# Performance work log

Hardware: AMD Instinct MI355X
Metric: run time of the kernel (lower is better)

Reference implementation:

```python
import jax, jax.numpy as jnp
import numpy as np

B, H, W, C = 4, 64, 64, 256


def _conv1x1(t, w, b):
    # 1x1 Conv2D == per-pixel matmul over channels (NHWC)
    return jnp.einsum('bhwc,cd->bhwd', t, w) + b


def setup_inputs() -> dict:
    key = jax.random.key(0)
    ks = jax.random.split(key, 12)
    s = 0.02
    inp = {
        'x': jax.random.normal(ks[0], (B, H, W, C), dtype=jnp.float32),
        'g': jax.random.normal(ks[1], (B, H, W, C), dtype=jnp.float32),
        'Wx1': jax.random.normal(ks[2], (C, C), dtype=jnp.float32) * s,
        'bx1': jnp.zeros((C,), dtype=jnp.float32),
        'Wx2': jax.random.normal(ks[3], (C, C), dtype=jnp.float32) * s,
        'bx2': jnp.zeros((C,), dtype=jnp.float32),
        'Wx3': jax.random.normal(ks[4], (C, C), dtype=jnp.float32) * s,
        'bx3': jnp.zeros((C,), dtype=jnp.float32),
        'Wg1': jax.random.normal(ks[5], (C, C), dtype=jnp.float32) * s,
        'bg1': jnp.zeros((C,), dtype=jnp.float32),
        'Wg2': jax.random.normal(ks[6], (C, C), dtype=jnp.float32) * s,
        'bg2': jnp.zeros((C,), dtype=jnp.float32),
    }
    return inp


def reference(x, g, Wx1, bx1, Wx2, bx2, Wx3, bx3, Wg1, bg1, Wg2, bg2):
    b, h, w, c = x.shape
    hw = h * w
    # x-branch projections, flattened to (B, HW, C)
    xw1 = _conv1x1(x, Wx1, bx1).reshape(b, hw, c)
    xw2 = _conv1x1(x, Wx2, bx2).reshape(b, hw, c)
    xw3 = _conv1x1(x, Wx3, bx3).reshape(b, hw, c)
    # g-branch projections
    gw1 = _conv1x1(g, Wg1, bg1).reshape(b, hw, c)
    gw2 = _conv1x1(g, Wg2, bg2).reshape(b, hw, c)
    # Dot(axes=(2,1))([xw_2, xw_1^T]) -> (B, HW, HW), softmax over last axis
    x_attn = jax.nn.softmax(jnp.einsum('bic,bjc->bij', xw2, xw1), axis=-1)
    g_attn = jax.nn.softmax(jnp.einsum('bic,bjc->bij', gw2, gw1), axis=-1)
    # elementwise gate then renormalize
    attn = jax.nn.softmax(x_attn * g_attn, axis=-1)
    # Keras Dot(axes=1): contract axis 1 of attn with axis 1 of xw3
    # out[b, j, c] = sum_i attn[b, i, j] * xw3[b, i, c]
    out = jnp.einsum('bij,bic->bjc', attn, xw3).reshape(b, h, w, c)
    return x + out
```

## Files before the change

### kernel.cpp

```cpp
#include <hip/hip_runtime.h>

typedef float f32x4 __attribute__((ext_vector_type(4)));
typedef short s16x8 __attribute__((ext_vector_type(8)));
typedef unsigned char u8;
typedef unsigned short u16;
typedef unsigned int u32;
typedef unsigned long long u64;

#define NPOS 4096
#define CCH  256
#define MTOT 16384
#define PBYTES ((size_t)NPOS * NPOS * 2)

#define SZ_F8   ((size_t)MTOT * 256)
#define O_F8    ((size_t)0)
#define O_WT    (O_F8   + 4 * SZ_F8)
#define O_XW3T  (O_WT   + (size_t)5*256*256*2)
#define O_XW3S  (O_XW3T + (size_t)MTOT*256*2)
#define O_ZX    (O_XW3S + (size_t)MTOT*256*2)
#define O_ZG    (O_ZX   + (size_t)8*MTOT*4)
#define O_ID    (O_ZG   + (size_t)8*MTOT*4)
#define O_Z2    (O_ID   + (size_t)MTOT*4)
#define O_IZ2   (O_Z2   + (size_t)8*MTOT*4)
#define O_P     (O_IZ2  + (size_t)MTOT*4)

__device__ __forceinline__ u16 f2bf(float f) {
    u32 u = __builtin_bit_cast(u32, f);
    u32 r = (u + 0x7FFFu + ((u >> 16) & 1u)) >> 16;
    return (u16)r;
}
__device__ __forceinline__ float bf2f(u16 h) {
    u32 u = ((u32)h) << 16;
    return __builtin_bit_cast(float, u);
}
__device__ __forceinline__ f32x4 mfma_bf16(s16x8 a, s16x8 b, f32x4 c) {
    return __builtin_amdgcn_mfma_f32_16x16x32_bf16(a, b, c, 0, 0, 0);
}
__device__ __forceinline__ f32x4 mfma_fp8(long a, long b, f32x4 c) {
    return __builtin_amdgcn_mfma_f32_16x16x32_fp8_fp8(a, b, c, 0, 0, 0);
}
__device__ __forceinline__ int xcd_swz(int bid, int nwg) {
    return (bid & 7) * (nwg >> 3) + (bid >> 3);
}

__global__ __launch_bounds__(256) void prep_w(
    const float* __restrict__ W0, const float* __restrict__ W1,
    const float* __restrict__ W2, const float* __restrict__ W3,
    const float* __restrict__ W4, u32* __restrict__ wT)
{
    const int p = blockIdx.x, kq = blockIdx.y, n = threadIdx.x;
    const float* W = (p==0)?W0:(p==1)?W1:(p==2)?W2:(p==3)?W3:W4;
#pragma unroll 4
    for (int kk = 0; kk < 32; ++kk) {
        int k = kq*64 + kk*2;
        float v0 = W[k*256 + n];
        float v1 = W[(k+1)*256 + n];
        wT[(p*65536 + n*256 + k) >> 1] = (u32)f2bf(v0) | ((u32)f2bf(v1) << 16);
    }
}

__global__ __launch_bounds__(256) void proj_kernel(
    const float* __restrict__ x, const float* __restrict__ g,
    const float* __restrict__ bb0, const float* __restrict__ bb1,
    const float* __restrict__ bb2, const float* __restrict__ bb3,
    const float* __restrict__ bb4,
    const u16* __restrict__ wT, u8* __restrict__ f8, u8* __restrict__ xw3T)
{
    const int branch = blockIdx.y;
    const int m0 = blockIdx.x * 128;
    const float* A = branch ? g : x;
    __shared__ u8 sA[128*512];
    __shared__ u8 sC[128*512];
    const int t = threadIdx.x;
    const int l = t & 63, lr = l & 15, lg = l >> 4;
    const int wv = t >> 6, wm = wv >> 1, wn = wv & 1;

    {
        const int m = t >> 1, h = t & 1;
        const float* src = &A[(size_t)(m0 + m) * 256 + h * 128];
        const u32 dbase = m * 512;
#pragma unroll
        for (int c = 0; c < 16; ++c) {
            float4 a = *(const float4*)(src + c*8);
            float4 b = *(const float4*)(src + c*8 + 4);
            u32 pk[4] = { (u32)f2bf(a.x) | ((u32)f2bf(a.y)<<16),
                          (u32)f2bf(a.z) | ((u32)f2bf(a.w)<<16),
                          (u32)f2bf(b.x) | ((u32)f2bf(b.y)<<16),
                          (u32)f2bf(b.z) | ((u32)f2bf(b.w)<<16) };
            int kbyte = h*256 + c*16;
            *(uint4*)&sA[dbase + (kbyte ^ ((m & 7) << 4))] = *(uint4*)pk;
        }
    }
    __syncthreads();

    const int np = branch ? 2 : 3;
    for (int pp = 0; pp < np; ++pp) {
        const int p = branch ? 3 + pp : pp;
        const float* bias = (p==0)?bb0:(p==1)?bb1:(p==2)?bb2:(p==3)?bb3:bb4;
        f32x4 acc[4][8];
#pragma unroll
        for (int i = 0; i < 4; ++i)
#pragma unroll
            for (int j = 0; j < 8; ++j) acc[i][j] = (f32x4){0.f,0.f,0.f,0.f};

#pragma unroll
        for (int ks = 0; ks < 8; ++ks) {
            s16x8 af[4];
#pragma unroll
            for (int Mt = 0; Mt < 4; ++Mt) {
                int m = wm*64 + Mt*16 + lr;
                af[Mt] = *(const s16x8*)&sA[m*512 + ((ks*64 + lg*16) ^ ((m & 7) << 4))];
            }
#pragma unroll
            for (int Nt = 0; Nt < 8; ++Nt) {
                int n = wn*128 + Nt*16 + lr;
                s16x8 bf = *(const s16x8*)&wT[p*65536 + n*256 + ks*32 + lg*8];
#pragma unroll
                for (int Mt = 0; Mt < 4; ++Mt)
                    acc[Mt][Nt] = mfma_bf16(af[Mt], bf, acc[Mt][Nt]);
            }
        }
#pragma unroll
        for (int Nt = 0; Nt < 8; ++Nt) {
            float bv = bias[wn*128 + Nt*16 + lr];
#pragma unroll
            for (int Mt = 0; Mt < 4; ++Mt)
#pragma unroll
                for (int q = 0; q < 4; ++q) acc[Mt][Nt][q] += bv;
        }

        if (p == 2) {
#pragma unroll
            for (int Mt = 0; Mt < 4; ++Mt)
#pragma unroll
                for (int Nt = 0; Nt < 8; ++Nt) {
                    int n = wn*128 + Nt*16 + lr;
                    int mrow = m0 + wm*64 + Mt*16 + lg*4;
                    int bb = mrow >> 12, pos = mrow & 4095;
                    uint2 val;
                    val.x = (u32)f2bf(acc[Mt][Nt][0]) | ((u32)f2bf(acc[Mt][Nt][1]) << 16);
                    val.y = (u32)f2bf(acc[Mt][Nt][2]) | ((u32)f2bf(acc[Mt][Nt][3]) << 16);
                    *(uint2*)(xw3T + ((size_t)(bb*256 + n)*4096 + pos)*2) = val;
                }
        } else {
            const int fi = (p < 2) ? p : p - 1;
#pragma unroll
            for (int Mt = 0; Mt < 4; ++Mt)
#pragma unroll
                for (int Nt = 0; Nt < 8; ++Nt) {
                    int n = wn*128 + Nt*16 + lr;
#pragma unroll
                    for (int q = 0; q < 4; ++q) {
                        int m = wm*64 + Mt*16 + lg*4 + q;
                        *(u16*)&sC[m*512 + ((n*2) ^ ((m & 7) << 4))] = f2bf(acc[Mt][Nt][q]);
                    }
                }
            __syncthreads();
            {
                const int m = t >> 1, h = t & 1;
                u8* dst = f8 + (size_t)fi * SZ_F8 + (size_t)(m0 + m)*256 + h*128;
#pragma unroll
                for (int c = 0; c < 16; ++c) {
                    uint4 v = *(const uint4*)&sC[m*512 + ((h*256 + c*16) ^ ((m & 7) << 4))];
                    float fv[8] = { bf2f((u16)(v.x & 0xffff)), bf2f((u16)(v.x >> 16)),
                                    bf2f((u16)(v.y & 0xffff)), bf2f((u16)(v.y >> 16)),
                                    bf2f((u16)(v.z & 0xffff)), bf2f((u16)(v.z >> 16)),
                                    bf2f((u16)(v.w & 0xffff)), bf2f((u16)(v.w >> 16)) };
                    u32 o0 = 0, o1 = 0;
                    o0 = __builtin_amdgcn_cvt_pk_fp8_f32(fv[0], fv[1], o0, false);
                    o0 = __builtin_amdgcn_cvt_pk_fp8_f32(fv[2], fv[3], o0, true);
                    o1 = __builtin_amdgcn_cvt_pk_fp8_f32(fv[4], fv[5], o1, false);
                    o1 = __builtin_amdgcn_cvt_pk_fp8_f32(fv[6], fv[7], o1, true);
                    uint2 ov; ov.x = o0; ov.y = o1;
                    *(uint2*)(dst + c*8) = ov;
                }
            }
            __syncthreads();
        }
    }
}

__global__ __launch_bounds__(256, 4) void stats1_kernel(
    const u8* __restrict__ f8, float* __restrict__ ZxP, float* __restrict__ ZgP)
{
    const int sid = xcd_swz(blockIdx.x, gridDim.x);
    const int b = sid >> 8, rem = sid & 255;
    const int iblk = rem & 31, js = rem >> 5;
    const int i0 = iblk * 128;
    const int t = threadIdx.x, l = t & 63, lr = l & 15, lg = l >> 4, w = t >> 6;
    const u8* Ax = f8 + SZ_F8*1 + ((size_t)(b*NPOS + i0 + w*32))*256;
    const u8* Ag = f8 + SZ_F8*3 + ((size_t)(b*NPOS + i0 + w*32))*256;
    const u8* Bx = f8 + SZ_F8*0 + ((size_t)(b*NPOS))*256;
    const u8* Bg = f8 + SZ_F8*2 + ((size_t)(b*NPOS))*256;

    long ax[2][8], ag[2][8];
#pragma unroll
    for (int Mt = 0; Mt < 2; ++Mt)
#pragma unroll
        for (int ks = 0; ks < 8; ++ks) {
            ax[Mt][ks] = *(const long*)&Ax[(Mt*16 + lr)*256 + ks*32 + lg*8];
            ag[Mt][ks] = *(const long*)&Ag[(Mt*16 + lr)*256 + ks*32 + lg*8];
        }

    float zx[2][4], zg[2][4];
#pragma unroll
    for (int Mt = 0; Mt < 2; ++Mt)
#pragma unroll
        for (int q = 0; q < 4; ++q) { zx[Mt][q] = 0.f; zg[Mt][q] = 0.f; }

    __shared__ __attribute__((aligned(16))) u8 sb[16384];
    for (int jc = 0; jc < 16; ++jc) {
        const int j0 = js*512 + jc*32;
#pragma unroll
        for (int rep = 0; rep < 4; ++rep) {
            int s = rep*256 + t;
            int br = s >> 9, s2 = s & 511;
            int jr = s2 >> 4, kb = (s2 & 15) << 4;
            const u8* src = (br ? Bg : Bx) + (size_t)(j0 + jr)*256 + kb;
            uint4 v = *(const uint4*)src;
            int a0 = br*8192 + jr*256 + (kb ^ ((jr & 15) << 3));
            *(u64*)&sb[a0]     = ((u64)v.y << 32) | v.x;
            *(u64*)&sb[a0 ^ 8] = ((u64)v.w << 32) | v.z;
        }
        __syncthreads();
        f32x4 cx[2][2], cg[2][2];
#pragma unroll
        for (int Mt = 0; Mt < 2; ++Mt)
#pragma unroll
            for (int jt = 0; jt < 2; ++jt) { cx[Mt][jt] = (f32x4){0,0,0,0}; cg[Mt][jt] = (f32x4){0,0,0,0}; }
#pragma unroll
        for (int ks = 0; ks < 8; ++ks)
#pragma unroll
            for (int jt = 0; jt < 2; ++jt) {
                int jrow = jt*16 + lr;
                int off = jrow*256 + ((ks*32 + lg*8) ^ ((jrow & 15) << 3));
                long bxv = *(const long*)&sb[off];
                long bgv = *(const long*)&sb[8192 + off];
#pragma unroll
                for (int Mt = 0; Mt < 2; ++Mt) {
                    cx[Mt][jt] = mfma_fp8(ax[Mt][ks], bxv, cx[Mt][jt]);
                    cg[Mt][jt] = mfma_fp8(ag[Mt][ks], bgv, cg[Mt][jt]);
                }
            }
        __syncthreads();
#pragma unroll
        for (int Mt = 0; Mt < 2; ++Mt)
#pragma unroll
            for (int jt = 0; jt < 2; ++jt)
#pragma unroll
                for (int q = 0; q < 4; ++q) {
                    zx[Mt][q] += __expf(cx[Mt][jt][q]);
                    zg[Mt][q] += __expf(cg[Mt][jt][q]);
                }
    }
#pragma unroll
    for (int Mt = 0; Mt < 2; ++Mt)
#pragma unroll
        for (int q = 0; q < 4; ++q)
#pragma unroll
            for (int o = 1; o < 16; o <<= 1) {
                zx[Mt][q] += __shfl_xor(zx[Mt][q], o, 64);
                zg[Mt][q] += __shfl_xor(zg[Mt][q], o, 64);
            }
    if (lr == 0) {
#pragma unroll
        for (int Mt = 0; Mt < 2; ++Mt)
#pragma unroll
            for (int q = 0; q < 4; ++q) {
                int gi = b*NPOS + i0 + w*32 + Mt*16 + lg*4 + q;
                ZxP[js*MTOT + gi] = zx[Mt][q];
                ZgP[js*MTOT + gi] = zg[Mt][q];
            }
    }
}

__global__ __launch_bounds__(256) void merge_d(
    const float* __restrict__ ZxP, const float* __restrict__ ZgP,
    float* __restrict__ iD)
{
    int gi = blockIdx.x*256 + threadIdx.x;
    float zx = 0.f, zg = 0.f;
#pragma unroll
    for (int js = 0; js < 8; ++js) { zx += ZxP[js*MTOT + gi]; zg += ZgP[js*MTOT + gi]; }
    iD[gi] = 1.0f / (zx * zg);
}

__global__ __launch_bounds__(256, 3) void stats2_kernel(
    const u8* __restrict__ f8, const float* __restrict__ iD,
    float* __restrict__ z2P, u8* __restrict__ PT, int bbase, int big)
{
    const int sid = xcd_swz(blockIdx.x, gridDim.x);
    const int bz = sid >> 8, rem = sid & 255;
    const int batch = bbase + bz;
    const int iblk = rem & 31, js = rem >> 5;
    const int i0 = iblk * 128;
    const int t = threadIdx.x, l = t & 63, lr = l & 15, lg = l >> 4, w = t >> 6;
    const u8* Ax = f8 + SZ_F8*1 + ((size_t)(batch*NPOS + i0 + w*32))*256;
    const u8* Ag = f8 + SZ_F8*3 + ((size_t)(batch*NPOS + i0 + w*32))*256;
    const u8* Bx = f8 + SZ_F8*0 + ((size_t)(batch*NPOS))*256;
    const u8* Bg = f8 + SZ_F8*2 + ((size_t)(batch*NPOS))*256;
    u8* PTb = PT + (big ? (size_t)bz * PBYTES : 0);

    long ax[2][8], ag[2][8];
#pragma unroll
    for (int Mt = 0; Mt < 2; ++Mt)
#pragma unroll
        for (int ks = 0; ks < 8; ++ks) {
            ax[Mt][ks] = *(const long*)&Ax[(Mt*16 + lr)*256 + ks*32 + lg*8];
            ag[Mt][ks] = *(const long*)&Ag[(Mt*16 + lr)*256 + ks*32 + lg*8];
        }
    f32x4 iDv[2];
#pragma unroll
    for (int Mt = 0; Mt < 2; ++Mt)
        iDv[Mt] = *(const f32x4*)&iD[batch*NPOS + i0 + w*32 + Mt*16 + lg*4];

    float z2a[2][4];
#pragma unroll
    for (int Mt = 0; Mt < 2; ++Mt)
#pragma unroll
        for (int q = 0; q < 4; ++q) z2a[Mt][q] = 0.f;

    __shared__ __attribute__((aligned(16))) u8 sb[16384];
    __shared__ __attribute__((aligned(16))) u8 pb[8192];
    for (int jc = 0; jc < 16; ++jc) {
        const int j0 = js*512 + jc*32;
#pragma unroll
        for (int rep = 0; rep < 4; ++rep) {
            int s = rep*256 + t;
            int br = s >> 9, s2 = s & 511;
            int jr = s2 >> 4, kb = (s2 & 15) << 4;
            const u8* src = (br ? Bg : Bx) + (size_t)(j0 + jr)*256 + kb;
            uint4 v = *(const uint4*)src;
            int a0 = br*8192 + jr*256 + (kb ^ ((jr & 15) << 3));
            *(u64*)&sb[a0]     = ((u64)v.y << 32) | v.x;
            *(u64*)&sb[a0 ^ 8] = ((u64)v.w << 32) | v.z;
        }
        __syncthreads();
        f32x4 cx[2][2], cg[2][2];
#pragma unroll
        for (int Mt = 0; Mt < 2; ++Mt)
#pragma unroll
            for (int jt = 0; jt < 2; ++jt) { cx[Mt][jt] = (f32x4){0,0,0,0}; cg[Mt][jt] = (f32x4){0,0,0,0}; }
#pragma unroll
        for (int ks = 0; ks < 8; ++ks)
#pragma unroll
            for (int jt = 0; jt < 2; ++jt) {
                int jrow = jt*16 + lr;
                int off = jrow*256 + ((ks*32 + lg*8) ^ ((jrow & 15) << 3));
                long bxv = *(const long*)&sb[off];
                long bgv = *(const long*)&sb[8192 + off];
#pragma unroll
                for (int Mt = 0; Mt < 2; ++Mt) {
                    cx[Mt][jt] = mfma_fp8(ax[Mt][ks], bxv, cx[Mt][jt]);
                    cg[Mt][jt] = mfma_fp8(ag[Mt][ks], bgv, cg[Mt][jt]);
                }
            }
#pragma unroll
        for (int Mt = 0; Mt < 2; ++Mt)
#pragma unroll
            for (int jt = 0; jt < 2; ++jt) {
                int jl = jt*16 + lr;
                float e[4];
#pragma unroll
                for (int q = 0; q < 4; ++q) {
                    float T = cx[Mt][jt][q] + cg[Mt][jt][q];
                    float v = __expf(T) * iDv[Mt][q];
                    e[q] = __expf(v);
                    z2a[Mt][q] += e[q];
                }
                u64 pk = (u64)((u32)f2bf(e[0]) | ((u32)f2bf(e[1]) << 16)) |
                         ((u64)((u32)f2bf(e[2]) | ((u32)f2bf(e[3]) << 16)) << 32);
                int ioff = w*64 + Mt*32 + lg*8;
                *(u64*)&pb[jl*256 + (ioff ^ ((jl & 15) << 3))] = pk;
            }
        __syncthreads();
        {
            const int row = t >> 3, seg = t & 7;
            const int swz = (row & 15) << 3;
            u8* dst = PTb + (size_t)(j0 + row)*8192 + (size_t)i0*2 + seg*32;
#pragma unroll
            for (int h = 0; h < 2; ++h) {
                int a0 = row*256 + ((seg*32 + h*16) ^ swz);
                u64 lo = *(const u64*)&pb[a0];
                u64 hi = *(const u64*)&pb[a0 ^ 8];
                uint4 o; o.x = (u32)lo; o.y = (u32)(lo >> 32);
                o.z = (u32)hi; o.w = (u32)(hi >> 32);
                *(uint4*)(dst + h*16) = o;
            }
        }
        __syncthreads();
    }
#pragma unroll
    for (int Mt = 0; Mt < 2; ++Mt)
#pragma unroll
        for (int q = 0; q < 4; ++q)
#pragma unroll
            for (int o = 1; o < 16; o <<= 1)
                z2a[Mt][q] += __shfl_xor(z2a[Mt][q], o, 64);
    if (lr == 0) {
#pragma unroll
        for (int Mt = 0; Mt < 2; ++Mt)
#pragma unroll
            for (int q = 0; q < 4; ++q) {
                int gi = batch*NPOS + i0 + w*32 + Mt*16 + lg*4 + q;
                z2P[js*MTOT + gi] = z2a[Mt][q];
            }
    }
}

__global__ __launch_bounds__(256) void prep_iz2(
    const float* __restrict__ z2P, float* __restrict__ iZ2, int bbase)
{
    int gi = bbase*NPOS + blockIdx.x*256 + threadIdx.x;
    float s = 0.f;
#pragma unroll
    for (int js = 0; js < 8; ++js) s += z2P[js*MTOT + gi];
    iZ2[gi] = 1.0f / s;
}

__global__ __launch_bounds__(256) void scalev(
    const u8* __restrict__ xw3T, const float* __restrict__ iZ2,
    u8* __restrict__ xw3s, int bbase)
{
    int eg = blockIdx.x*256 + threadIdx.x;
    int bz = bbase + (eg >> 17);
    int rem = eg & 131071;
    int c = rem >> 9, i = (rem & 511) << 3;
    size_t off = ((size_t)(bz*256 + c)*4096 + i)*2;
    uint4 v = *(const uint4*)(xw3T + off);
    f32x4 z0 = *(const f32x4*)&iZ2[bz*NPOS + i];
    f32x4 z1 = *(const f32x4*)&iZ2[bz*NPOS + i + 4];
    uint4 r;
    r.x = (u32)f2bf(bf2f((u16)(v.x & 0xffff))*z0[0]) | ((u32)f2bf(bf2f((u16)(v.x >> 16))*z0[1]) << 16);
    r.y = (u32)f2bf(bf2f((u16)(v.y & 0xffff))*z0[2]) | ((u32)f2bf(bf2f((u16)(v.y >> 16))*z0[3]) << 16);
    r.z = (u32)f2bf(bf2f((u16)(v.z & 0xffff))*z1[0]) | ((u32)f2bf(bf2f((u16)(v.z >> 16))*z1[1]) << 16);
    r.w = (u32)f2bf(bf2f((u16)(v.w & 0xffff))*z1[2]) | ((u32)f2bf(bf2f((u16)(v.w >> 16))*z1[3]) << 16);
    *(uint4*)(xw3s + off) = r;
}

__global__ __launch_bounds__(256, 4) void pv_kernel(
    const u8* __restrict__ PT, const u8* __restrict__ xw3s,
    const float* __restrict__ x, float* __restrict__ out, int bbase, int big)
{
    const int sid = xcd_swz(blockIdx.x, gridDim.x);
    const int bz = sid >> 8, rem = sid & 255;
    const int batch = bbase + bz;
    const int j0 = (rem & 63) * 64, c0 = (rem >> 6) * 64;
    const u8* PTb = PT + (big ? (size_t)bz * PBYTES : 0);
    __shared__ __attribute__((aligned(16))) u8 sA[8192], sB[8192];
    const int t = threadIdx.x, l = t & 63, lr = l & 15, lg = l >> 4;
    const int wv = t >> 6, wm = wv >> 1, wn = wv & 1;

    f32x4 acc[2][2];
#pragma unroll
    for (int Mt = 0; Mt < 2; ++Mt)
#pragma unroll
        for (int Nt = 0; Nt < 2; ++Nt) acc[Mt][Nt] = (f32x4){0,0,0,0};

    for (int kt = 0; kt < 64; ++kt) {
        const int k0 = kt * 64;
#pragma unroll
        for (int rep = 0; rep < 4; ++rep) {
            int s = rep*256 + t;
            int buf = s >> 9, s2 = s & 511;
            int row = s2 >> 3, seg = s2 & 7;
            const u8* src = buf
                ? xw3s + ((size_t)(batch*256 + c0 + row)*4096 + k0)*2 + seg*16
                : PTb  + ((size_t)(j0 + row)*4096 + k0)*2 + seg*16;
            u8* dst = (buf ? sB : sA) + row*128 + ((seg*16) ^ ((row & 7) << 4));
            *(uint4*)dst = *(const uint4*)src;
        }
        __syncthreads();
#pragma unroll
        for (int ks = 0; ks < 2; ++ks) {
            s16x8 af[2], bf[2];
#pragma unroll
            for (int Mt = 0; Mt < 2; ++Mt) {
                int row = wm*32 + Mt*16 + lr;
                af[Mt] = *(const s16x8*)&sA[row*128 + ((ks*64 + lg*16) ^ ((row & 7) << 4))];
            }
#pragma unroll
            for (int Nt = 0; Nt < 2; ++Nt) {
                int row = wn*32 + Nt*16 + lr;
                bf[Nt] = *(const s16x8*)&sB[row*128 + ((ks*64 + lg*16) ^ ((row & 7) << 4))];
            }
#pragma unroll
            for (int Mt = 0; Mt < 2; ++Mt)
#pragma unroll
                for (int Nt = 0; Nt < 2; ++Nt)
                    acc[Mt][Nt] = mfma_bf16(af[Mt], bf[Nt], acc[Mt][Nt]);
        }
        __syncthreads();
    }
#pragma unroll
    for (int Mt = 0; Mt < 2; ++Mt)
#pragma unroll
        for (int Nt = 0; Nt < 2; ++Nt)
#pragma unroll
            for (int q = 0; q < 4; ++q) {
                int j = j0 + wm*32 + Mt*16 + lg*4 + q;
                int c = c0 + wn*32 + Nt*16 + lr;
                size_t idx = ((size_t)(batch*NPOS + j))*256 + c;
                out[idx] = x[idx] + acc[Mt][Nt][q];
            }
}

extern "C" void kernel_launch(void* const* d_in, const int* in_sizes, int n_in,
                              void* d_out, int out_size, void* d_ws, size_t ws_size,
                              hipStream_t stream)
{
    const float* x = (const float*)d_in[0];
    const float* g = (const float*)d_in[1];
    const float* W[5]  = {(const float*)d_in[2], (const float*)d_in[4], (const float*)d_in[6],
                          (const float*)d_in[8], (const float*)d_in[10]};
    const float* Bi[5] = {(const float*)d_in[3], (const float*)d_in[5], (const float*)d_in[7],
                          (const float*)d_in[9], (const float*)d_in[11]};
    char* ws = (char*)d_ws;
    u8*  f8   = (u8*)(ws + O_F8);
    u16* wT   = (u16*)(ws + O_WT);
    u8*  xw3T = (u8*)(ws + O_XW3T);
    u8*  xw3s = (u8*)(ws + O_XW3S);
    float* ZxP = (float*)(ws + O_ZX);
    float* ZgP = (float*)(ws + O_ZG);
    float* iD  = (float*)(ws + O_ID);
    float* z2P = (float*)(ws + O_Z2);
    float* iZ2 = (float*)(ws + O_IZ2);
    u8*  PT   = (u8*)(ws + O_P);
    float* out = (float*)d_out;

    const int big = (ws_size >= O_P + 4 * PBYTES) ? 1 : 0;

    prep_w<<<dim3(5,4), 256, 0, stream>>>(W[0], W[1], W[2], W[3], W[4], (u32*)wT);
    proj_kernel<<<dim3(128,2), 256, 0, stream>>>(x, g, Bi[0], Bi[1], Bi[2], Bi[3], Bi[4],
                                                 wT, f8, xw3T);
    stats1_kernel<<<1024, 256, 0, stream>>>(f8, ZxP, ZgP);
    merge_d<<<64, 256, 0, stream>>>(ZxP, ZgP, iD);
    if (big) {
        stats2_kernel<<<1024, 256, 0, stream>>>(f8, iD, z2P, PT, 0, 1);
        prep_iz2<<<64, 256, 0, stream>>>(z2P, iZ2, 0);
        scalev<<<2048, 256, 0, stream>>>(xw3T, iZ2, xw3s, 0);
        pv_kernel<<<1024, 256, 0, stream>>>(PT, xw3s, x, out, 0, 1);
    } else {
        for (int b = 0; b < 4; ++b) {
            stats2_kernel<<<256, 256, 0, stream>>>(f8, iD, z2P, PT, b, 0);
            prep_iz2<<<16, 256, 0, stream>>>(z2P, iZ2, b);
            scalev<<<512, 256, 0, stream>>>(xw3T, iZ2, xw3s, b);
            pv_kernel<<<256, 256, 0, stream>>>(PT, xw3s, x, out, b, 0);
        }
    }
}
```

Baseline: 306.2 us.

## Compute score matrix once, defer row normalization to a separate pass

Removes the standalone stats1 pass that recomputed both fp8 QK^T products just to get the softmax denominators. The score kernel now stores the unnormalized product exp(sx)*exp(sg) while accumulating both row sums. A new zpass kernel rereads the stored matrix to build the second-softmax denominator, and the PV kernel applies the normalizations and exp on the fly, with a wider 256-channel tile that replaces the separate scalev kernel. In exchange it adds an extra full read of the large probability matrix, stores the unnormalized product in bf16 (a possible range and precision concern), and does more exp work inside the PV loads.

```diff
diff --git a/kernel.cpp b/kernel.cpp
--- a/kernel.cpp
+++ b/kernel.cpp
@@ -16,12 +16,11 @@
 #define O_F8    ((size_t)0)
 #define O_WT    (O_F8   + 4 * SZ_F8)
 #define O_XW3T  (O_WT   + (size_t)5*256*256*2)
-#define O_XW3S  (O_XW3T + (size_t)MTOT*256*2)
-#define O_ZX    (O_XW3S + (size_t)MTOT*256*2)
+#define O_ZX    (O_XW3T + (size_t)MTOT*256*2)
 #define O_ZG    (O_ZX   + (size_t)8*MTOT*4)
 #define O_ID    (O_ZG   + (size_t)8*MTOT*4)
 #define O_Z2    (O_ID   + (size_t)MTOT*4)
-#define O_IZ2   (O_Z2   + (size_t)8*MTOT*4)
+#define O_IZ2   (O_Z2   + (size_t)64*MTOT*4)
 #define O_P     (O_IZ2  + (size_t)MTOT*4)
 
 __device__ __forceinline__ u16 f2bf(float f) {
@@ -32,6 +31,9 @@
 __device__ __forceinline__ float bf2f(u16 h) {
     u32 u = ((u32)h) << 16;
     return __builtin_bit_cast(float, u);
+}
+__device__ __forceinline__ u32 pk2(float a, float b) {
+    return (u32)f2bf(a) | ((u32)f2bf(b) << 16);
 }
 __device__ __forceinline__ f32x4 mfma_bf16(s16x8 a, s16x8 b, f32x4 c) {
     return __builtin_amdgcn_mfma_f32_16x16x32_bf16(a, b, c, 0, 0, 0);
@@ -55,7 +57,7 @@
         int k = kq*64 + kk*2;
         float v0 = W[k*256 + n];
         float v1 = W[(k+1)*256 + n];
-        wT[(p*65536 + n*256 + k) >> 1] = (u32)f2bf(v0) | ((u32)f2bf(v1) << 16);
+        wT[(p*65536 + n*256 + k) >> 1] = pk2(v0, v1);
     }
 }
 
@@ -83,10 +85,7 @@
         for (int c = 0; c < 16; ++c) {
             float4 a = *(const float4*)(src + c*8);
             float4 b = *(const float4*)(src + c*8 + 4);
-            u32 pk[4] = { (u32)f2bf(a.x) | ((u32)f2bf(a.y)<<16),
-                          (u32)f2bf(a.z) | ((u32)f2bf(a.w)<<16),
-                          (u32)f2bf(b.x) | ((u32)f2bf(b.y)<<16),
-                          (u32)f2bf(b.z) | ((u32)f2bf(b.w)<<16) };
+            u32 pk[4] = { pk2(a.x, a.y), pk2(a.z, a.w), pk2(b.x, b.y), pk2(b.z, b.w) };
             int kbyte = h*256 + c*16;
             *(uint4*)&sA[dbase + (kbyte ^ ((m & 7) << 4))] = *(uint4*)pk;
         }
@@ -138,8 +137,8 @@
                     int mrow = m0 + wm*64 + Mt*16 + lg*4;
                     int bb = mrow >> 12, pos = mrow & 4095;
                     uint2 val;
-                    val.x = (u32)f2bf(acc[Mt][Nt][0]) | ((u32)f2bf(acc[Mt][Nt][1]) << 16);
-                    val.y = (u32)f2bf(acc[Mt][Nt][2]) | ((u32)f2bf(acc[Mt][Nt][3]) << 16);
+                    val.x = pk2(acc[Mt][Nt][0], acc[Mt][Nt][1]);
+                    val.y = pk2(acc[Mt][Nt][2], acc[Mt][Nt][3]);
                     *(uint2*)(xw3T + ((size_t)(bb*256 + n)*4096 + pos)*2) = val;
                 }
         } else {
@@ -180,114 +179,9 @@
     }
 }
 
-__global__ __launch_bounds__(256, 4) void stats1_kernel(
-    const u8* __restrict__ f8, float* __restrict__ ZxP, float* __restrict__ ZgP)
-{
-    const int sid = xcd_swz(blockIdx.x, gridDim.x);
-    const int b = sid >> 8, rem = sid & 255;
-    const int iblk = rem & 31, js = rem >> 5;
-    const int i0 = iblk * 128;
-    const int t = threadIdx.x, l = t & 63, lr = l & 15, lg = l >> 4, w = t >> 6;
-    const u8* Ax = f8 + SZ_F8*1 + ((size_t)(b*NPOS + i0 + w*32))*256;
-    const u8* Ag = f8 + SZ_F8*3 + ((size_t)(b*NPOS + i0 + w*32))*256;
-    const u8* Bx = f8 + SZ_F8*0 + ((size_t)(b*NPOS))*256;
-    const u8* Bg = f8 + SZ_F8*2 + ((size_t)(b*NPOS))*256;
-
-    long ax[2][8], ag[2][8];
-#pragma unroll
-    for (int Mt = 0; Mt < 2; ++Mt)
-#pragma unroll
-        for (int ks = 0; ks < 8; ++ks) {
-            ax[Mt][ks] = *(const long*)&Ax[(Mt*16 + lr)*256 + ks*32 + lg*8];
-            ag[Mt][ks] = *(const long*)&Ag[(Mt*16 + lr)*256 + ks*32 + lg*8];
-        }
-
-    float zx[2][4], zg[2][4];
-#pragma unroll
-    for (int Mt = 0; Mt < 2; ++Mt)
-#pragma unroll
-        for (int q = 0; q < 4; ++q) { zx[Mt][q] = 0.f; zg[Mt][q] = 0.f; }
-
-    __shared__ __attribute__((aligned(16))) u8 sb[16384];
-    for (int jc = 0; jc < 16; ++jc) {
-        const int j0 = js*512 + jc*32;
-#pragma unroll
-        for (int rep = 0; rep < 4; ++rep) {
-            int s = rep*256 + t;
-            int br = s >> 9, s2 = s & 511;
-            int jr = s2 >> 4, kb = (s2 & 15) << 4;
-            const u8* src = (br ? Bg : Bx) + (size_t)(j0 + jr)*256 + kb;
-            uint4 v = *(const uint4*)src;
-            int a0 = br*8192 + jr*256 + (kb ^ ((jr & 15) << 3));
-            *(u64*)&sb[a0]     = ((u64)v.y << 32) | v.x;
-            *(u64*)&sb[a0 ^ 8] = ((u64)v.w << 32) | v.z;
-        }
-        __syncthreads();
-        f32x4 cx[2][2], cg[2][2];
-#pragma unroll
-        for (int Mt = 0; Mt < 2; ++Mt)
-#pragma unroll
-            for (int jt = 0; jt < 2; ++jt) { cx[Mt][jt] = (f32x4){0,0,0,0}; cg[Mt][jt] = (f32x4){0,0,0,0}; }
-#pragma unroll
-        for (int ks = 0; ks < 8; ++ks)
-#pragma unroll
-            for (int jt = 0; jt < 2; ++jt) {
-                int jrow = jt*16 + lr;
-                int off = jrow*256 + ((ks*32 + lg*8) ^ ((jrow & 15) << 3));
-                long bxv = *(const long*)&sb[off];
-                long bgv = *(const long*)&sb[8192 + off];
-#pragma unroll
-                for (int Mt = 0; Mt < 2; ++Mt) {
-                    cx[Mt][jt] = mfma_fp8(ax[Mt][ks], bxv, cx[Mt][jt]);
-                    cg[Mt][jt] = mfma_fp8(ag[Mt][ks], bgv, cg[Mt][jt]);
-                }
-            }
-        __syncthreads();
-#pragma unroll
-        for (int Mt = 0; Mt < 2; ++Mt)
-#pragma unroll
-            for (int jt = 0; jt < 2; ++jt)
-#pragma unroll
-                for (int q = 0; q < 4; ++q) {
-                    zx[Mt][q] += __expf(cx[Mt][jt][q]);
-                    zg[Mt][q] += __expf(cg[Mt][jt][q]);
-                }
-    }
-#pragma unroll
-    for (int Mt = 0; Mt < 2; ++Mt)
-#pragma unroll
-        for (int q = 0; q < 4; ++q)
-#pragma unroll
-            for (int o = 1; o < 16; o <<= 1) {
-                zx[Mt][q] += __shfl_xor(zx[Mt][q], o, 64);
-                zg[Mt][q] += __shfl_xor(zg[Mt][q], o, 64);
-            }
-    if (lr == 0) {
-#pragma unroll
-        for (int Mt = 0; Mt < 2; ++Mt)
-#pragma unroll
-            for (int q = 0; q < 4; ++q) {
-                int gi = b*NPOS + i0 + w*32 + Mt*16 + lg*4 + q;
-                ZxP[js*MTOT + gi] = zx[Mt][q];
-                ZgP[js*MTOT + gi] = zg[Mt][q];
-            }
-    }
-}
-
-__global__ __launch_bounds__(256) void merge_d(
-    const float* __restrict__ ZxP, const float* __restrict__ ZgP,
-    float* __restrict__ iD)
-{
-    int gi = blockIdx.x*256 + threadIdx.x;
-    float zx = 0.f, zg = 0.f;
-#pragma unroll
-    for (int js = 0; js < 8; ++js) { zx += ZxP[js*MTOT + gi]; zg += ZgP[js*MTOT + gi]; }
-    iD[gi] = 1.0f / (zx * zg);
-}
-
-__global__ __launch_bounds__(256, 3) void stats2_kernel(
-    const u8* __restrict__ f8, const float* __restrict__ iD,
-    float* __restrict__ z2P, u8* __restrict__ PT, int bbase, int big)
+__global__ __launch_bounds__(256, 3) void score_kernel(
+    const u8* __restrict__ f8, float* __restrict__ ZxP, float* __restrict__ ZgP,
+    u8* __restrict__ PT, int bbase, int big)
 {
     const int sid = xcd_swz(blockIdx.x, gridDim.x);
     const int bz = sid >> 8, rem = sid & 255;
@@ -309,16 +203,12 @@
             ax[Mt][ks] = *(const long*)&Ax[(Mt*16 + lr)*256 + ks*32 + lg*8];
             ag[Mt][ks] = *(const long*)&Ag[(Mt*16 + lr)*256 + ks*32 + lg*8];
         }
-    f32x4 iDv[2];
+
+    float zx[2][4], zg[2][4];
 #pragma unroll
     for (int Mt = 0; Mt < 2; ++Mt)
-        iDv[Mt] = *(const f32x4*)&iD[batch*NPOS + i0 + w*32 + Mt*16 + lg*4];
-
-    float z2a[2][4];
-#pragma unroll
-    for (int Mt = 0; Mt < 2; ++Mt)
-#pragma unroll
-        for (int q = 0; q < 4; ++q) z2a[Mt][q] = 0.f;
+#pragma unroll
+        for (int q = 0; q < 4; ++q) { zx[Mt][q] = 0.f; zg[Mt][q] = 0.f; }
 
     __shared__ __attribute__((aligned(16))) u8 sb[16384];
     __shared__ __attribute__((aligned(16))) u8 pb[8192];
@@ -363,13 +253,13 @@
                 float e[4];
 #pragma unroll
                 for (int q = 0; q < 4; ++q) {
-                    float T = cx[Mt][jt][q] + cg[Mt][jt][q];
-                    float v = __expf(T) * iDv[Mt][q];
-                    e[q] = __expf(v);
-                    z2a[Mt][q] += e[q];
+                    float exv = __expf(cx[Mt][jt][q]);
+                    float egv = __expf(cg[Mt][jt][q]);
+                    zx[Mt][q] += exv;
+                    zg[Mt][q] += egv;
+                    e[q] = exv * egv;
                 }
-                u64 pk = (u64)((u32)f2bf(e[0]) | ((u32)f2bf(e[1]) << 16)) |
-                         ((u64)((u32)f2bf(e[2]) | ((u32)f2bf(e[3]) << 16)) << 32);
+                u64 pk = (u64)pk2(e[0], e[1]) | ((u64)pk2(e[2], e[3]) << 32);
                 int ioff = w*64 + Mt*32 + lg*8;
                 *(u64*)&pb[jl*256 + (ioff ^ ((jl & 15) << 3))] = pk;
             }
@@ -395,17 +285,61 @@
 #pragma unroll
         for (int q = 0; q < 4; ++q)
 #pragma unroll
-            for (int o = 1; o < 16; o <<= 1)
-                z2a[Mt][q] += __shfl_xor(z2a[Mt][q], o, 64);
+            for (int o = 1; o < 16; o <<= 1) {
+                zx[Mt][q] += __shfl_xor(zx[Mt][q], o, 64);
+                zg[Mt][q] += __shfl_xor(zg[Mt][q], o, 64);
+            }
     if (lr == 0) {
 #pragma unroll
         for (int Mt = 0; Mt < 2; ++Mt)
 #pragma unroll
             for (int q = 0; q < 4; ++q) {
                 int gi = batch*NPOS + i0 + w*32 + Mt*16 + lg*4 + q;
-                z2P[js*MTOT + gi] = z2a[Mt][q];
-            }
-    }
+                ZxP[js*MTOT + gi] = zx[Mt][q];
+                ZgP[js*MTOT + gi] = zg[Mt][q];
+            }
+    }
+}
+
+__global__ __launch_bounds__(256) void merge_d(
+    const float* __restrict__ ZxP, const float* __restrict__ ZgP,
+    float* __restrict__ iD, int bbase)
+{
+    int gi = bbase*NPOS + blockIdx.x*256 + threadIdx.x;
+    float zx = 0.f, zg = 0.f;
+#pragma unroll
+    for (int js = 0; js < 8; ++js) { zx += ZxP[js*MTOT + gi]; zg += ZgP[js*MTOT + gi]; }
+    iD[gi] = 1.0f / (zx * zg);
+}
+
+__global__ __launch_bounds__(256) void zpass_kernel(
+    const u8* __restrict__ PT, const float* __restrict__ iD,
+    float* __restrict__ z2P, int bbase, int big)
+{
+    const int sid = xcd_swz(blockIdx.x, gridDim.x);
+    const int bz = sid >> 7, r = sid & 127;
+    const int ih = r >> 6, js = r & 63;
+    const int batch = bbase + bz;
+    const u8* base = PT + (big ? (size_t)bz * PBYTES : 0) + (size_t)(js*64)*8192;
+    const int i = ih*2048 + threadIdx.x*8;
+    f32x4 d0 = *(const f32x4*)&iD[batch*NPOS + i];
+    f32x4 d1 = *(const f32x4*)&iD[batch*NPOS + i + 4];
+    f32x4 z0 = (f32x4){0,0,0,0}, z1 = (f32x4){0,0,0,0};
+#pragma unroll 4
+    for (int jr = 0; jr < 64; ++jr) {
+        uint4 v = *(const uint4*)(base + (size_t)jr*8192 + (size_t)i*2);
+        z0[0] += __expf(bf2f((u16)(v.x & 0xffff)) * d0[0]);
+        z0[1] += __expf(bf2f((u16)(v.x >> 16))    * d0[1]);
+        z0[2] += __expf(bf2f((u16)(v.y & 0xffff)) * d0[2]);
+        z0[3] += __expf(bf2f((u16)(v.y >> 16))    * d0[3]);
+        z1[0] += __expf(bf2f((u16)(v.z & 0xffff)) * d1[0]);
+        z1[1] += __expf(bf2f((u16)(v.z >> 16))    * d1[1]);
+        z1[2] += __expf(bf2f((u16)(v.w & 0xffff)) * d1[2]);
+        z1[3] += __expf(bf2f((u16)(v.w >> 16))    * d1[3]);
+    }
+    float* dst = z2P + (size_t)js*MTOT + batch*NPOS + i;
+    *(f32x4*)dst = z0;
+    *(f32x4*)(dst + 4) = z1;
 }
 
 __global__ __launch_bounds__(256) void prep_iz2(
@@ -413,93 +347,95 @@
 {
     int gi = bbase*NPOS + blockIdx.x*256 + threadIdx.x;
     float s = 0.f;
-#pragma unroll
-    for (int js = 0; js < 8; ++js) s += z2P[js*MTOT + gi];
+#pragma unroll 8
+    for (int js = 0; js < 64; ++js) s += z2P[js*MTOT + gi];
     iZ2[gi] = 1.0f / s;
 }
 
-__global__ __launch_bounds__(256) void scalev(
-    const u8* __restrict__ xw3T, const float* __restrict__ iZ2,
-    u8* __restrict__ xw3s, int bbase)
-{
-    int eg = blockIdx.x*256 + threadIdx.x;
-    int bz = bbase + (eg >> 17);
-    int rem = eg & 131071;
-    int c = rem >> 9, i = (rem & 511) << 3;
-    size_t off = ((size_t)(bz*256 + c)*4096 + i)*2;
-    uint4 v = *(const uint4*)(xw3T + off);
-    f32x4 z0 = *(const f32x4*)&iZ2[bz*NPOS + i];
-    f32x4 z1 = *(const f32x4*)&iZ2[bz*NPOS + i + 4];
-    uint4 r;
-    r.x = (u32)f2bf(bf2f((u16)(v.x & 0xffff))*z0[0]) | ((u32)f2bf(bf2f((u16)(v.x >> 16))*z0[1]) << 16);
-    r.y = (u32)f2bf(bf2f((u16)(v.y & 0xffff))*z0[2]) | ((u32)f2bf(bf2f((u16)(v.y >> 16))*z0[3]) << 16);
-    r.z = (u32)f2bf(bf2f((u16)(v.z & 0xffff))*z1[0]) | ((u32)f2bf(bf2f((u16)(v.z >> 16))*z1[1]) << 16);
-    r.w = (u32)f2bf(bf2f((u16)(v.w & 0xffff))*z1[2]) | ((u32)f2bf(bf2f((u16)(v.w >> 16))*z1[3]) << 16);
-    *(uint4*)(xw3s + off) = r;
-}
-
-__global__ __launch_bounds__(256, 4) void pv_kernel(
-    const u8* __restrict__ PT, const u8* __restrict__ xw3s,
+__global__ __launch_bounds__(256, 2) void pv_kernel(
+    const u8* __restrict__ PT, const u8* __restrict__ xw3T,
+    const float* __restrict__ iD, const float* __restrict__ iZ2,
     const float* __restrict__ x, float* __restrict__ out, int bbase, int big)
 {
     const int sid = xcd_swz(blockIdx.x, gridDim.x);
-    const int bz = sid >> 8, rem = sid & 255;
+    const int bz = sid >> 6, jb = sid & 63;
     const int batch = bbase + bz;
-    const int j0 = (rem & 63) * 64, c0 = (rem >> 6) * 64;
+    const int j0 = jb * 64;
     const u8* PTb = PT + (big ? (size_t)bz * PBYTES : 0);
-    __shared__ __attribute__((aligned(16))) u8 sA[8192], sB[8192];
+    const u8* xw3Tb = xw3T + (size_t)batch * 256 * 4096 * 2;
+    const float* iDb = iD + batch*NPOS;
+    const float* iZb = iZ2 + batch*NPOS;
+    __shared__ __attribute__((aligned(16))) u8 sA[8192];
+    __shared__ __attribute__((aligned(16))) u8 sB[32768];
     const int t = threadIdx.x, l = t & 63, lr = l & 15, lg = l >> 4;
     const int wv = t >> 6, wm = wv >> 1, wn = wv & 1;
 
-    f32x4 acc[2][2];
+    f32x4 acc[2][8];
 #pragma unroll
     for (int Mt = 0; Mt < 2; ++Mt)
 #pragma unroll
-        for (int Nt = 0; Nt < 2; ++Nt) acc[Mt][Nt] = (f32x4){0,0,0,0};
+        for (int Nt = 0; Nt < 8; ++Nt) acc[Mt][Nt] = (f32x4){0,0,0,0};
 
     for (int kt = 0; kt < 64; ++kt) {
         const int k0 = kt * 64;
 #pragma unroll
-        for (int rep = 0; rep < 4; ++rep) {
+        for (int rep = 0; rep < 2; ++rep) {
             int s = rep*256 + t;
-            int buf = s >> 9, s2 = s & 511;
-            int row = s2 >> 3, seg = s2 & 7;
-            const u8* src = buf
-                ? xw3s + ((size_t)(batch*256 + c0 + row)*4096 + k0)*2 + seg*16
-                : PTb  + ((size_t)(j0 + row)*4096 + k0)*2 + seg*16;
-            u8* dst = (buf ? sB : sA) + row*128 + ((seg*16) ^ ((row & 7) << 4));
-            *(uint4*)dst = *(const uint4*)src;
+            int row = s >> 3, seg = s & 7;
+            int ib = k0 + seg*8;
+            uint4 v = *(const uint4*)(PTb + (size_t)(j0 + row)*8192 + (size_t)ib*2);
+            f32x4 d0 = *(const f32x4*)&iDb[ib];
+            f32x4 d1 = *(const f32x4*)&iDb[ib + 4];
+            uint4 o;
+            o.x = pk2(__expf(bf2f((u16)(v.x & 0xffff))*d0[0]), __expf(bf2f((u16)(v.x >> 16))*d0[1]));
+            o.y = pk2(__expf(bf2f((u16)(v.y & 0xffff))*d0[2]), __expf(bf2f((u16)(v.y >> 16))*d0[3]));
+            o.z = pk2(__expf(bf2f((u16)(v.z & 0xffff))*d1[0]), __expf(bf2f((u16)(v.z >> 16))*d1[1]));
+            o.w = pk2(__expf(bf2f((u16)(v.w & 0xffff))*d1[2]), __expf(bf2f((u16)(v.w >> 16))*d1[3]));
+            *(uint4*)&sA[row*128 + ((seg*16) ^ ((row & 7) << 4))] = o;
+        }
+#pragma unroll
+        for (int rep = 0; rep < 8; ++rep) {
+            int s = rep*256 + t;
+            int row = s >> 3, seg = s & 7;
+            int ib = k0 + seg*8;
+            uint4 v = *(const uint4*)(xw3Tb + ((size_t)row*4096 + ib)*2);
+            f32x4 d0 = *(const f32x4*)&iZb[ib];
+            f32x4 d1 = *(const f32x4*)&iZb[ib + 4];
+            uint4 o;
+            o.x = pk2(bf2f((u16)(v.x & 0xffff))*d0[0], bf2f((u16)(v.x >> 16))*d0[1]);
+            o.y = pk2(bf2f((u16)(v.y & 0xffff))*d0[2], bf2f((u16)(v.y >> 16))*d0[3]);
+            o.z = pk2(bf2f((u16)(v.z & 0xffff))*d1[0], bf2f((u16)(v.z >> 16))*d1[1]);
+            o.w = pk2(bf2f((u16)(v.w & 0xffff))*d1[2], bf2f((u16)(v.w >> 16))*d1[3]);
+            *(uint4*)&sB[row*128 + ((seg*16) ^ ((row & 7) << 4))] = o;
         }
         __syncthreads();
 #pragma unroll
         for (int ks = 0; ks < 2; ++ks) {
-            s16x8 af[2], bf[2];
+            s16x8 af[2];
 #pragma unroll
             for (int Mt = 0; Mt < 2; ++Mt) {
                 int row = wm*32 + Mt*16 + lr;
                 af[Mt] = *(const s16x8*)&sA[row*128 + ((ks*64 + lg*16) ^ ((row & 7) << 4))];
             }
 #pragma unroll
-            for (int Nt = 0; Nt < 2; ++Nt) {
-                int row = wn*32 + Nt*16 + lr;
-                bf[Nt] = *(const s16x8*)&sB[row*128 + ((ks*64 + lg*16) ^ ((row & 7) << 4))];
-            }
-#pragma unroll
-            for (int Mt = 0; Mt < 2; ++Mt)
-#pragma unroll
-                for (int Nt = 0; Nt < 2; ++Nt)
-                    acc[Mt][Nt] = mfma_bf16(af[Mt], bf[Nt], acc[Mt][Nt]);
+            for (int Nt = 0; Nt < 8; ++Nt) {
+                int row = wn*128 + Nt*16 + lr;
+                s16x8 bf = *(const s16x8*)&sB[row*128 + ((ks*64 + lg*16) ^ ((row & 7) << 4))];
+#pragma unroll
+                for (int Mt = 0; Mt < 2; ++Mt)
+                    acc[Mt][Nt] = mfma_bf16(af[Mt], bf, acc[Mt][Nt]);
+            }
         }
         __syncthreads();
     }
 #pragma unroll
     for (int Mt = 0; Mt < 2; ++Mt)
 #pragma unroll
-        for (int Nt = 0; Nt < 2; ++Nt)
+        for (int Nt = 0; Nt < 8; ++Nt)
 #pragma unroll
             for (int q = 0; q < 4; ++q) {
                 int j = j0 + wm*32 + Mt*16 + lg*4 + q;
-                int c = c0 + wn*32 + Nt*16 + lr;
+                int c = wn*128 + Nt*16 + lr;
                 size_t idx = ((size_t)(batch*NPOS + j))*256 + c;
                 out[idx] = x[idx] + acc[Mt][Nt][q];
             }
@@ -519,7 +455,6 @@
     u8*  f8   = (u8*)(ws + O_F8);
     u16* wT   = (u16*)(ws + O_WT);
     u8*  xw3T = (u8*)(ws + O_XW3T);
-    u8*  xw3s = (u8*)(ws + O_XW3S);
     float* ZxP = (float*)(ws + O_ZX);
     float* ZgP = (float*)(ws + O_ZG);
     float* iD  = (float*)(ws + O_ID);
@@ -533,19 +468,19 @@
     prep_w<<<dim3(5,4), 256, 0, stream>>>(W[0], W[1], W[2], W[3], W[4], (u32*)wT);
     proj_kernel<<<dim3(128,2), 256, 0, stream>>>(x, g, Bi[0], Bi[1], Bi[2], Bi[3], Bi[4],
                                                  wT, f8, xw3T);
-    stats1_kernel<<<1024, 256, 0, stream>>>(f8, ZxP, ZgP);
-    merge_d<<<64, 256, 0, stream>>>(ZxP, ZgP, iD);
     if (big) {
-        stats2_kernel<<<1024, 256, 0, stream>>>(f8, iD, z2P, PT, 0, 1);
+        score_kernel<<<1024, 256, 0, stream>>>(f8, ZxP, ZgP, PT, 0, 1);
+        merge_d<<<64, 256, 0, stream>>>(ZxP, ZgP, iD, 0);
+        zpass_kernel<<<512, 256, 0, stream>>>(PT, iD, z2P, 0, 1);
         prep_iz2<<<64, 256, 0, stream>>>(z2P, iZ2, 0);
-        scalev<<<2048, 256, 0, stream>>>(xw3T, iZ2, xw3s, 0);
-        pv_kernel<<<1024, 256, 0, stream>>>(PT, xw3s, x, out, 0, 1);
+        pv_kernel<<<256, 256, 0, stream>>>(PT, xw3T, iD, iZ2, x, out, 0, 1);
     } else {
         for (int b = 0; b < 4; ++b) {
-            stats2_kernel<<<256, 256, 0, stream>>>(f8, iD, z2P, PT, b, 0);
+            score_kernel<<<256, 256, 0, stream>>>(f8, ZxP, ZgP, PT, b, 0);
+            merge_d<<<16, 256, 0, stream>>>(ZxP, ZgP, iD, b);
+            zpass_kernel<<<128, 256, 0, stream>>>(PT, iD, z2P, b, 0);
             prep_iz2<<<16, 256, 0, stream>>>(z2P, iZ2, b);
-            scalev<<<512, 256, 0, stream>>>(xw3T, iZ2, xw3s, b);
-            pv_kernel<<<256, 256, 0, stream>>>(PT, xw3s, x, out, b, 0);
-        }
-    }
-}
+            pv_kernel<<<64, 256, 0, stream>>>(PT, xw3T, iD, iZ2, x, out, b, 0);
+        }
+    }
+}
```

Result: slower. 474.6 us (+55.0%).
